# Optimization experiments

Measured on AMD Instinct MI355X. Metric: run time of the kernel, lower is better.

## Reference

```python
import jax, jax.numpy as jnp
import numpy as np

HEAD_NUM = 8
QKV_DIM = 16
EMB = 128
SQRT_EMB = 11.313708498984761  # sqrt(128)
LOGIT_CLIP = 10.0


def _heads(x):
    # (B, n, H*d) -> (B, H, n, d)
    B, n, _ = x.shape
    return x.reshape(B, n, HEAD_NUM, QKV_DIM).transpose(0, 2, 1, 3)


def _mha(q, k, v, rank3_ninf_mask):
    # q: (B,H,n,d), k/v: (B,H,m,d), mask: (B,n,m)
    score = jnp.einsum('bhnd,bhmd->bhnm', q, k) / jnp.sqrt(jnp.float32(QKV_DIM))
    score = score + rank3_ninf_mask[:, None, :, :]
    w = jax.nn.softmax(score, axis=3)
    out = jnp.einsum('bhnm,bhmd->bhnd', w, v)
    B, H, n, d = out.shape
    return out.transpose(0, 2, 1, 3).reshape(B, n, H * d)


def setup_inputs() -> dict:
    key = jax.random.key(0)
    ks = jax.random.split(key, 20)
    B, N, P = 32, 512, 512
    s = 1.0 / np.sqrt(EMB)
    inp = {
        'encoded_nodes': jax.random.normal(ks[0], (B, N, EMB), jnp.float32),
        'encoded_graph': jax.random.normal(ks[1], (B, N, EMB), jnp.float32),
        'encoded_q1': jax.random.normal(ks[2], (B, P, EMB), jnp.float32),
        'encoded_first_graph': jax.random.normal(ks[3], (B, P, EMB), jnp.float32),
        'encoded_last_node': jax.random.normal(ks[4], (B, P, EMB), jnp.float32),
        'encoded_last_graph': jax.random.normal(ks[5], (B, P, EMB), jnp.float32),
        'ninf_mask': jnp.zeros((B, P, N), jnp.float32),
        # weights stored (in, out); torch Linear y = x @ W.T
        'Wq_first': jax.random.uniform(ks[6], (EMB, EMB), jnp.float32, -s, s),
        'Wq_last': jax.random.uniform(ks[7], (EMB, EMB), jnp.float32, -s, s),
        'Wk': jax.random.uniform(ks[8], (EMB, EMB), jnp.float32, -s, s),
        'Wv': jax.random.uniform(ks[9], (EMB, EMB), jnp.float32, -s, s),
        'Wq_first_e': jax.random.uniform(ks[10], (EMB, EMB), jnp.float32, -s, s),
        'Wq_last_e': jax.random.uniform(ks[11], (EMB, EMB), jnp.float32, -s, s),
        'Wk_e': jax.random.uniform(ks[12], (EMB, EMB), jnp.float32, -s, s),
        'Wv_e': jax.random.uniform(ks[13], (EMB, EMB), jnp.float32, -s, s),
        'Wcomb1': jax.random.uniform(ks[14], (EMB, EMB), jnp.float32, -s, s),
        'bcomb1': jax.random.uniform(ks[15], (EMB,), jnp.float32, -s, s),
        'Wcomb2': jax.random.uniform(ks[16], (EMB, EMB), jnp.float32, -s, s),
        'bcomb2': jax.random.uniform(ks[17], (EMB,), jnp.float32, -s, s),
    }
    return inp


def reference(encoded_nodes, encoded_graph, encoded_q1, encoded_first_graph,
              encoded_last_node, encoded_last_graph, ninf_mask,
              Wq_first, Wq_last, Wk, Wv,
              Wq_first_e, Wq_last_e, Wk_e, Wv_e,
              Wcomb1, bcomb1, Wcomb2, bcomb2):
    # set_kv
    k = _heads(encoded_nodes @ Wk)
    v = _heads(encoded_nodes @ Wv)
    k_e = _heads(encoded_graph @ Wk_e)
    v_e = _heads(encoded_graph @ Wv_e)
    # set_q1
    q_first = _heads(encoded_q1 @ Wq_first)
    q_first_e = _heads(encoded_first_graph @ Wq_first_e)
    # forward
    q_last = _heads(encoded_last_node @ Wq_last)
    q_last_e = _heads(encoded_last_graph @ Wq_last_e)
    q = (q_first + q_last) + (q_first_e + q_last_e)
    out1 = _mha(q, k, v, ninf_mask)
    out2 = _mha(q, k_e, v_e, ninf_mask)
    mh_out = (out1 @ Wcomb1 + bcomb1) + (out2 @ Wcomb2 + bcomb2)
    # single-head scoring against summed keys: (B,n,e) x (B,N,e) -> (B,n,N)
    shk = encoded_nodes + encoded_graph
    score = jnp.einsum('bne,bNe->bnN', mh_out, shk) / SQRT_EMB
    score = LOGIT_CLIP * jnp.tanh(score) + ninf_mask
    probs = jax.nn.softmax(score, axis=2)
    return probs
```

## Files before the change

kernel.cpp:

```cpp
#include <hip/hip_runtime.h>

#define BATCH 32
#define SEQ   512
#define EMBD  128
#define HEADS 8
#define HD    16
#define ROWS  (BATCH*SEQ)
#define GR    32
#define NT32  (ROWS/GR)

__device__ __forceinline__ void gemm_nolds(const float* __restrict__ A,
                                           const float* __restrict__ W,
                                           int rowBase, int tid,
                                           float acc[4][4])
{
    const int r0 = (tid >> 5) * 4;
    const int c0 = (tid & 31) * 4;
    const float* Ab = A + (size_t)(rowBase + r0) * EMBD;
    for (int e0 = 0; e0 < EMBD; e0 += 4) {
        float4 a[4];
        #pragma unroll
        for (int r = 0; r < 4; ++r)
            a[r] = *(const float4*)(Ab + r*EMBD + e0);
        float4 w[4];
        #pragma unroll
        for (int j = 0; j < 4; ++j)
            w[j] = *(const float4*)(W + (e0+j)*EMBD + c0);
        #pragma unroll
        for (int r = 0; r < 4; ++r) {
            acc[r][0] += a[r].x*w[0].x + a[r].y*w[1].x + a[r].z*w[2].x + a[r].w*w[3].x;
            acc[r][1] += a[r].x*w[0].y + a[r].y*w[1].y + a[r].z*w[2].y + a[r].w*w[3].y;
            acc[r][2] += a[r].x*w[0].z + a[r].y*w[1].z + a[r].z*w[2].z + a[r].w*w[3].z;
            acc[r][3] += a[r].x*w[0].w + a[r].y*w[1].w + a[r].z*w[2].w + a[r].w*w[3].w;
        }
    }
}

__device__ __forceinline__ void store_nolds(float* __restrict__ out,
                                            int rowBase, int tid,
                                            float acc[4][4])
{
    const int r0 = (tid >> 5) * 4;
    const int c0 = (tid & 31) * 4;
    #pragma unroll
    for (int r = 0; r < 4; ++r)
        *(float4*)(out + (size_t)(rowBase + r0 + r)*EMBD + c0) =
            make_float4(acc[r][0], acc[r][1], acc[r][2], acc[r][3]);
}

__global__ __launch_bounds__(256) void proj_all_kernel(
    const float* __restrict__ nodes, const float* __restrict__ graph,
    const float* __restrict__ q1,    const float* __restrict__ fg,
    const float* __restrict__ ln,    const float* __restrict__ lg,
    const float* __restrict__ Wqf,  const float* __restrict__ Wql,
    const float* __restrict__ Wqfe, const float* __restrict__ Wqle,
    const float* __restrict__ Wk,   const float* __restrict__ Wv,
    const float* __restrict__ Wke,  const float* __restrict__ Wve,
    float* __restrict__ Qb, float* __restrict__ Kb, float* __restrict__ Vb,
    float* __restrict__ Keb, float* __restrict__ Veb)
{
    const int tid = threadIdx.x;
    const int rowBase = blockIdx.x * GR;
    const int job = blockIdx.y;
    float acc[4][4];
    #pragma unroll
    for (int r = 0; r < 4; ++r)
        #pragma unroll
        for (int c = 0; c < 4; ++c) acc[r][c] = 0.f;
    if (job == 0) {
        gemm_nolds(q1, Wqf,  rowBase, tid, acc);
        gemm_nolds(ln, Wql,  rowBase, tid, acc);
        gemm_nolds(fg, Wqfe, rowBase, tid, acc);
        gemm_nolds(lg, Wqle, rowBase, tid, acc);
        store_nolds(Qb, rowBase, tid, acc);
    } else if (job == 1) {
        gemm_nolds(nodes, Wk, rowBase, tid, acc);
        store_nolds(Kb, rowBase, tid, acc);
    } else if (job == 2) {
        gemm_nolds(nodes, Wv, rowBase, tid, acc);
        store_nolds(Vb, rowBase, tid, acc);
    } else if (job == 3) {
        gemm_nolds(graph, Wke, rowBase, tid, acc);
        store_nolds(Keb, rowBase, tid, acc);
    } else {
        gemm_nolds(graph, Wve, rowBase, tid, acc);
        store_nolds(Veb, rowBase, tid, acc);
    }
}

__global__ __launch_bounds__(256) void combine_kernel(
    const float* __restrict__ A0, const float* __restrict__ W0,
    const float* __restrict__ A1, const float* __restrict__ W1,
    const float* __restrict__ b0, const float* __restrict__ b1,
    float* __restrict__ out)
{
    const int tid = threadIdx.x;
    const int rowBase = blockIdx.x * GR;
    const int c0 = (tid & 31) * 4;
    float acc[4][4];
    #pragma unroll
    for (int c = 0; c < 4; ++c) {
        float bv = b0[c0+c] + b1[c0+c];
        #pragma unroll
        for (int r = 0; r < 4; ++r) acc[r][c] = bv;
    }
    gemm_nolds(A0, W0, rowBase, tid, acc);
    gemm_nolds(A1, W1, rowBase, tid, acc);
    store_nolds(out, rowBase, tid, acc);
}

__global__ __launch_bounds__(1024) void attn_kernel(
    const float* __restrict__ Qm, const float* __restrict__ Km,
    const float* __restrict__ Vm, const float* __restrict__ Kem,
    const float* __restrict__ Vem, const float* __restrict__ mask,
    float* __restrict__ out1, float* __restrict__ out2)
{
    extern __shared__ float smem[];
    float4* sK0 = (float4*)smem;
    float4* sV0 = sK0 + 2048;
    float4* sK1 = sV0 + 2048;
    float4* sV1 = sK1 + 2048;
    const int tid  = threadIdx.x;
    const int b    = blockIdx.x & 31;
    const int j    = blockIdx.x >> 5;
    const int type = j & 1;
    const int hp   = j >> 1;
    const float* K = type ? Kem : Km;
    const float* V = type ? Vem : Vm;
    float* outp    = type ? out2 : out1;
    const int h0 = hp * 2;
    {
        const float4* K4 = (const float4*)K;
        const float4* V4 = (const float4*)V;
        const int b0 = b*(SEQ*EMBD/4) + h0*(HD/4);
        #pragma unroll
        for (int k = 0; k < 2; ++k) {
            int i = tid + k*1024;
            int m = i >> 2, jj = i & 3;
            int g0 = b0 + m*(EMBD/4) + jj;
            sK0[i] = K4[g0];
            sV0[i] = V4[g0];
            sK1[i] = K4[g0 + 4];
            sV1[i] = V4[g0 + 4];
        }
    }
    __syncthreads();

    const int head = tid >> 9;
    const int row  = tid & 511;
    const float4* sK = head ? sK1 : sK0;
    const float4* sV = head ? sV1 : sV0;

    float q[16];
    {
        const float4* Q4 = (const float4*)Qm;
        const int qb = b*(SEQ*EMBD/4) + row*(EMBD/4) + (h0+head)*(HD/4);
        #pragma unroll
        for (int jj = 0; jj < 4; ++jj)
            *(float4*)&q[jj*4] = Q4[qb + jj];
    }
    const float4* mrow4 = (const float4*)(mask + ((size_t)b*SEQ + row)*SEQ);

    float l = 0.f;
    float acc[16];
    #pragma unroll
    for (int d = 0; d < 16; ++d) acc[d] = 0.f;

    for (int mc = 0; mc < SEQ/16; ++mc) {
        float4 mk[4];
        #pragma unroll
        for (int k = 0; k < 4; ++k) mk[k] = mrow4[mc*4 + k];
        const float* mkf = (const float*)mk;
        #pragma unroll
        for (int u = 0; u < 16; ++u) {
            const int m = mc*16 + u;
            float4 k0 = sK[m*4+0], k1 = sK[m*4+1], k2 = sK[m*4+2], k3 = sK[m*4+3];
            float s = q[0]*k0.x + q[1]*k0.y + q[2]*k0.z + q[3]*k0.w
                    + q[4]*k1.x + q[5]*k1.y + q[6]*k1.z + q[7]*k1.w
                    + q[8]*k2.x + q[9]*k2.y + q[10]*k2.z + q[11]*k2.w
                    + q[12]*k3.x + q[13]*k3.y + q[14]*k3.z + q[15]*k3.w;
            float p = __expf(s*0.25f + mkf[u]);
            l += p;
            float4 v0 = sV[m*4+0], v1 = sV[m*4+1], v2 = sV[m*4+2], v3 = sV[m*4+3];
            acc[0]+=p*v0.x;  acc[1]+=p*v0.y;  acc[2]+=p*v0.z;  acc[3]+=p*v0.w;
            acc[4]+=p*v1.x;  acc[5]+=p*v1.y;  acc[6]+=p*v1.z;  acc[7]+=p*v1.w;
            acc[8]+=p*v2.x;  acc[9]+=p*v2.y;  acc[10]+=p*v2.z; acc[11]+=p*v2.w;
            acc[12]+=p*v3.x; acc[13]+=p*v3.y; acc[14]+=p*v3.z; acc[15]+=p*v3.w;
        }
    }
    const float inv = 1.f / l;
    float4* o4 = (float4*)outp;
    const int ob = b*(SEQ*EMBD/4) + row*(EMBD/4) + (h0+head)*(HD/4);
    #pragma unroll
    for (int jj = 0; jj < 4; ++jj)
        o4[ob + jj] = make_float4(acc[jj*4]*inv, acc[jj*4+1]*inv,
                                  acc[jj*4+2]*inv, acc[jj*4+3]*inv);
}

#define RB 32
#define MT 64
__global__ __launch_bounds__(512) void final_kernel(
    const float* __restrict__ mh, const float* __restrict__ nodes,
    const float* __restrict__ graph, const float* __restrict__ mask,
    float* __restrict__ out)
{
    extern __shared__ float smem[];
    float4* sShk4 = (float4*)smem;
    float*  sMh   = smem + MT*EMBD;
    const int tid  = threadIdx.x;
    const int b    = blockIdx.x & 31;
    const int row0 = (blockIdx.x >> 5) * RB;
    const int mg = tid & 63;
    const int rg = tid >> 6;

    {
        const float4* mh4 = (const float4*)(mh + ((size_t)b*SEQ + row0)*EMBD);
        ((float4*)sMh)[tid]       = mh4[tid];
        ((float4*)sMh)[tid + 512] = mh4[tid + 512];
    }

    const float4* n4 = (const float4*)nodes;
    const float4* g4 = (const float4*)graph;
    float p[4][8];
    float rs[4] = {0.f, 0.f, 0.f, 0.f};

    #pragma unroll
    for (int mt = 0; mt < SEQ/MT; ++mt) {
        const int m0 = mt * MT;
        __syncthreads();
        {
            const int gb = (b*SEQ + m0) * (EMBD/4);
            #pragma unroll
            for (int k = 0; k < 4; ++k) {
                int i = tid + k*512;
                int m = i >> 5, f = i & 31;
                float4 x = n4[gb + m*32 + f];
                float4 y = g4[gb + m*32 + f];
                float4 s4;
                s4.x = x.x + y.x; s4.y = x.y + y.y;
                s4.z = x.z + y.z; s4.w = x.w + y.w;
                sShk4[(m << 5) | (f ^ (m & 31))] = s4;
            }
        }
        __syncthreads();

        float acc[4] = {0.f, 0.f, 0.f, 0.f};
        const int m = mg;
        #pragma unroll 8
        for (int e0 = 0; e0 < EMBD; e0 += 4) {
            const int f = e0 >> 2;
            float4 s = sShk4[(m << 5) | (f ^ (m & 31))];
            #pragma unroll
            for (int r = 0; r < 4; ++r) {
                const float* a = &sMh[(rg*4+r)*EMBD + e0];
                acc[r] += a[0]*s.x + a[1]*s.y + a[2]*s.z + a[3]*s.w;
            }
        }
        #pragma unroll
        for (int r = 0; r < 4; ++r) {
            const int row = row0 + rg*4 + r;
            float x = acc[r] * 0.088388347648318447f;
            float t = 1.f - 2.f / (__expf(2.f*x) + 1.f);
            float sc = 10.f*t + mask[((size_t)b*SEQ + row)*SEQ + m0 + mg];
            float pp = __expf(sc);
            p[r][mt] = pp;
            rs[r] += pp;
        }
    }

    #pragma unroll
    for (int r = 0; r < 4; ++r) {
        float s = rs[r];
        #pragma unroll
        for (int off = 32; off >= 1; off >>= 1) s += __shfl_xor(s, off);
        rs[r] = 1.f / s;
    }

    #pragma unroll
    for (int mt = 0; mt < SEQ/MT; ++mt) {
        #pragma unroll
        for (int r = 0; r < 4; ++r) {
            const int row = row0 + rg*4 + r;
            out[((size_t)b*SEQ + row)*SEQ + mt*MT + mg] = p[r][mt] * rs[r];
        }
    }
}

extern "C" void kernel_launch(void* const* d_in, const int* in_sizes, int n_in,
                              void* d_out, int out_size, void* d_ws, size_t ws_size,
                              hipStream_t stream)
{
    const float* nodes = (const float*)d_in[0];
    const float* graph = (const float*)d_in[1];
    const float* q1    = (const float*)d_in[2];
    const float* fg    = (const float*)d_in[3];
    const float* ln    = (const float*)d_in[4];
    const float* lg    = (const float*)d_in[5];
    const float* mask  = (const float*)d_in[6];
    const float* Wqf   = (const float*)d_in[7];
    const float* Wql   = (const float*)d_in[8];
    const float* Wk    = (const float*)d_in[9];
    const float* Wv    = (const float*)d_in[10];
    const float* Wqfe  = (const float*)d_in[11];
    const float* Wqle  = (const float*)d_in[12];
    const float* Wke   = (const float*)d_in[13];
    const float* Wve   = (const float*)d_in[14];
    const float* Wc1   = (const float*)d_in[15];
    const float* bc1   = (const float*)d_in[16];
    const float* Wc2   = (const float*)d_in[17];
    const float* bc2   = (const float*)d_in[18];

    float* ws = (float*)d_ws;
    const size_t BUF = (size_t)ROWS * EMBD;
    float* Qb  = ws;
    float* Kb  = ws + BUF;
    float* Vb  = ws + 2*BUF;
    float* Keb = ws + 3*BUF;
    float* Veb = ws + 4*BUF;
    float* mhb = Qb;
    float* o1  = (float*)d_out;
    float* o2  = o1 + BUF;

    const int LDS_ATTN  = 4 * SEQ * HD * 4;
    const int LDS_FINAL = (MT*EMBD + RB*EMBD) * 4;
    hipFuncSetAttribute((const void*)attn_kernel,  hipFuncAttributeMaxDynamicSharedMemorySize, LDS_ATTN);
    hipFuncSetAttribute((const void*)final_kernel, hipFuncAttributeMaxDynamicSharedMemorySize, LDS_FINAL);

    proj_all_kernel<<<dim3(NT32, 5), 256, 0, stream>>>(
        nodes, graph, q1, fg, ln, lg,
        Wqf, Wql, Wqfe, Wqle, Wk, Wv, Wke, Wve,
        Qb, Kb, Vb, Keb, Veb);
    attn_kernel<<<BATCH*8, 1024, LDS_ATTN, stream>>>(
        Qb, Kb, Vb, Keb, Veb, mask, o1, o2);
    combine_kernel<<<NT32, 256, 0, stream>>>(
        o1, Wc1, o2, Wc2, bc1, bc2, mhb);
    final_kernel<<<BATCH*(SEQ/RB), 512, LDS_FINAL, stream>>>(
        mhb, nodes, graph, mask, (float*)d_out);
}
```

Measured before the change: 547.7 us.

## Compute two query rows per thread in attention and two key columns in final

The attention kernel now runs 512 threads per block, and each thread handles two query rows, so every K/V value read from LDS is reused twice. The final kernel doubles its key tile to 128 and has each thread compute two key columns, so each mh value read from LDS is reused twice. Both changes cut LDS traffic per FLOP. The cost is roughly doubled accumulator registers and fewer threads per block in attention, which may reduce occupancy and latency hiding.

```diff
diff --git a/kernel.cpp b/kernel.cpp
--- a/kernel.cpp
+++ b/kernel.cpp
@@ -109,7 +109,7 @@
     store_nolds(out, rowBase, tid, acc);
 }
 
-__global__ __launch_bounds__(1024) void attn_kernel(
+__global__ __launch_bounds__(512) void attn_kernel(
     const float* __restrict__ Qm, const float* __restrict__ Km,
     const float* __restrict__ Vm, const float* __restrict__ Kem,
     const float* __restrict__ Vem, const float* __restrict__ mask,
@@ -134,8 +134,8 @@
         const float4* V4 = (const float4*)V;
         const int b0 = b*(SEQ*EMBD/4) + h0*(HD/4);
         #pragma unroll
-        for (int k = 0; k < 2; ++k) {
-            int i = tid + k*1024;
+        for (int k = 0; k < 4; ++k) {
+            int i = tid + k*512;
             int m = i >> 2, jj = i & 3;
             int g0 = b0 + m*(EMBD/4) + jj;
             sK0[i] = K4[g0];
@@ -146,59 +146,83 @@
     }
     __syncthreads();
 
-    const int head = tid >> 9;
-    const int row  = tid & 511;
+    const int head = tid >> 8;
+    const int r0   = tid & 255;
     const float4* sK = head ? sK1 : sK0;
     const float4* sV = head ? sV1 : sV0;
 
-    float q[16];
+    float q[2][16];
     {
         const float4* Q4 = (const float4*)Qm;
-        const int qb = b*(SEQ*EMBD/4) + row*(EMBD/4) + (h0+head)*(HD/4);
-        #pragma unroll
-        for (int jj = 0; jj < 4; ++jj)
-            *(float4*)&q[jj*4] = Q4[qb + jj];
-    }
-    const float4* mrow4 = (const float4*)(mask + ((size_t)b*SEQ + row)*SEQ);
-
-    float l = 0.f;
-    float acc[16];
-    #pragma unroll
-    for (int d = 0; d < 16; ++d) acc[d] = 0.f;
+        #pragma unroll
+        for (int rr = 0; rr < 2; ++rr) {
+            const int qb = b*(SEQ*EMBD/4) + (r0 + rr*256)*(EMBD/4) + (h0+head)*(HD/4);
+            #pragma unroll
+            for (int jj = 0; jj < 4; ++jj)
+                *(float4*)&q[rr][jj*4] = Q4[qb + jj];
+        }
+    }
+    const float4* mrowA = (const float4*)(mask + ((size_t)b*SEQ + r0)*SEQ);
+    const float4* mrowB = (const float4*)(mask + ((size_t)b*SEQ + r0 + 256)*SEQ);
+
+    float l0 = 0.f, l1 = 0.f;
+    float acc0[16], acc1[16];
+    #pragma unroll
+    for (int d = 0; d < 16; ++d) { acc0[d] = 0.f; acc1[d] = 0.f; }
 
     for (int mc = 0; mc < SEQ/16; ++mc) {
-        float4 mk[4];
-        #pragma unroll
-        for (int k = 0; k < 4; ++k) mk[k] = mrow4[mc*4 + k];
-        const float* mkf = (const float*)mk;
+        float4 mkA[4], mkB[4];
+        #pragma unroll
+        for (int k = 0; k < 4; ++k) { mkA[k] = mrowA[mc*4 + k]; mkB[k] = mrowB[mc*4 + k]; }
+        const float* mfA = (const float*)mkA;
+        const float* mfB = (const float*)mkB;
         #pragma unroll
         for (int u = 0; u < 16; ++u) {
             const int m = mc*16 + u;
             float4 k0 = sK[m*4+0], k1 = sK[m*4+1], k2 = sK[m*4+2], k3 = sK[m*4+3];
-            float s = q[0]*k0.x + q[1]*k0.y + q[2]*k0.z + q[3]*k0.w
-                    + q[4]*k1.x + q[5]*k1.y + q[6]*k1.z + q[7]*k1.w
-                    + q[8]*k2.x + q[9]*k2.y + q[10]*k2.z + q[11]*k2.w
-                    + q[12]*k3.x + q[13]*k3.y + q[14]*k3.z + q[15]*k3.w;
-            float p = __expf(s*0.25f + mkf[u]);
-            l += p;
+            float s0 = q[0][0]*k0.x + q[0][1]*k0.y + q[0][2]*k0.z + q[0][3]*k0.w
+                     + q[0][4]*k1.x + q[0][5]*k1.y + q[0][6]*k1.z + q[0][7]*k1.w
+                     + q[0][8]*k2.x + q[0][9]*k2.y + q[0][10]*k2.z + q[0][11]*k2.w
+                     + q[0][12]*k3.x + q[0][13]*k3.y + q[0][14]*k3.z + q[0][15]*k3.w;
+            float s1 = q[1][0]*k0.x + q[1][1]*k0.y + q[1][2]*k0.z + q[1][3]*k0.w
+                     + q[1][4]*k1.x + q[1][5]*k1.y + q[1][6]*k1.z + q[1][7]*k1.w
+                     + q[1][8]*k2.x + q[1][9]*k2.y + q[1][10]*k2.z + q[1][11]*k2.w
+                     + q[1][12]*k3.x + q[1][13]*k3.y + q[1][14]*k3.z + q[1][15]*k3.w;
+            float p0 = __expf(s0*0.25f + mfA[u]);
+            float p1 = __expf(s1*0.25f + mfB[u]);
+            l0 += p0; l1 += p1;
             float4 v0 = sV[m*4+0], v1 = sV[m*4+1], v2 = sV[m*4+2], v3 = sV[m*4+3];
-            acc[0]+=p*v0.x;  acc[1]+=p*v0.y;  acc[2]+=p*v0.z;  acc[3]+=p*v0.w;
-            acc[4]+=p*v1.x;  acc[5]+=p*v1.y;  acc[6]+=p*v1.z;  acc[7]+=p*v1.w;
-            acc[8]+=p*v2.x;  acc[9]+=p*v2.y;  acc[10]+=p*v2.z; acc[11]+=p*v2.w;
-            acc[12]+=p*v3.x; acc[13]+=p*v3.y; acc[14]+=p*v3.z; acc[15]+=p*v3.w;
-        }
-    }
-    const float inv = 1.f / l;
+            acc0[0]+=p0*v0.x;  acc0[1]+=p0*v0.y;  acc0[2]+=p0*v0.z;  acc0[3]+=p0*v0.w;
+            acc0[4]+=p0*v1.x;  acc0[5]+=p0*v1.y;  acc0[6]+=p0*v1.z;  acc0[7]+=p0*v1.w;
+            acc0[8]+=p0*v2.x;  acc0[9]+=p0*v2.y;  acc0[10]+=p0*v2.z; acc0[11]+=p0*v2.w;
+            acc0[12]+=p0*v3.x; acc0[13]+=p0*v3.y; acc0[14]+=p0*v3.z; acc0[15]+=p0*v3.w;
+            acc1[0]+=p1*v0.x;  acc1[1]+=p1*v0.y;  acc1[2]+=p1*v0.z;  acc1[3]+=p1*v0.w;
+            acc1[4]+=p1*v1.x;  acc1[5]+=p1*v1.y;  acc1[6]+=p1*v1.z;  acc1[7]+=p1*v1.w;
+            acc1[8]+=p1*v2.x;  acc1[9]+=p1*v2.y;  acc1[10]+=p1*v2.z; acc1[11]+=p1*v2.w;
+            acc1[12]+=p1*v3.x; acc1[13]+=p1*v3.y; acc1[14]+=p1*v3.z; acc1[15]+=p1*v3.w;
+        }
+    }
     float4* o4 = (float4*)outp;
-    const int ob = b*(SEQ*EMBD/4) + row*(EMBD/4) + (h0+head)*(HD/4);
-    #pragma unroll
-    for (int jj = 0; jj < 4; ++jj)
-        o4[ob + jj] = make_float4(acc[jj*4]*inv, acc[jj*4+1]*inv,
-                                  acc[jj*4+2]*inv, acc[jj*4+3]*inv);
+    const float i0 = 1.f / l0;
+    const float i1 = 1.f / l1;
+    {
+        const int ob = b*(SEQ*EMBD/4) + r0*(EMBD/4) + (h0+head)*(HD/4);
+        #pragma unroll
+        for (int jj = 0; jj < 4; ++jj)
+            o4[ob + jj] = make_float4(acc0[jj*4]*i0, acc0[jj*4+1]*i0,
+                                      acc0[jj*4+2]*i0, acc0[jj*4+3]*i0);
+    }
+    {
+        const int ob = b*(SEQ*EMBD/4) + (r0+256)*(EMBD/4) + (h0+head)*(HD/4);
+        #pragma unroll
+        for (int jj = 0; jj < 4; ++jj)
+            o4[ob + jj] = make_float4(acc1[jj*4]*i1, acc1[jj*4+1]*i1,
+                                      acc1[jj*4+2]*i1, acc1[jj*4+3]*i1);
+    }
 }
 
 #define RB 32
-#define MT 64
+#define MT 128
 __global__ __launch_bounds__(512) void final_kernel(
     const float* __restrict__ mh, const float* __restrict__ nodes,
     const float* __restrict__ graph, const float* __restrict__ mask,
@@ -231,7 +255,7 @@
         {
             const int gb = (b*SEQ + m0) * (EMBD/4);
             #pragma unroll
-            for (int k = 0; k < 4; ++k) {
+            for (int k = 0; k < 8; ++k) {
                 int i = tid + k*512;
                 int m = i >> 5, f = i & 31;
                 float4 x = n4[gb + m*32 + f];
@@ -244,27 +268,35 @@
         }
         __syncthreads();
 
-        float acc[4] = {0.f, 0.f, 0.f, 0.f};
-        const int m = mg;
+        float acc[4][2];
+        #pragma unroll
+        for (int r = 0; r < 4; ++r) { acc[r][0] = 0.f; acc[r][1] = 0.f; }
+        const int mA = mg, mB = mg + 64;
         #pragma unroll 8
         for (int e0 = 0; e0 < EMBD; e0 += 4) {
             const int f = e0 >> 2;
-            float4 s = sShk4[(m << 5) | (f ^ (m & 31))];
+            float4 s0 = sShk4[(mA << 5) | (f ^ (mA & 31))];
+            float4 s1 = sShk4[(mB << 5) | (f ^ (mB & 31))];
             #pragma unroll
             for (int r = 0; r < 4; ++r) {
                 const float* a = &sMh[(rg*4+r)*EMBD + e0];
-                acc[r] += a[0]*s.x + a[1]*s.y + a[2]*s.z + a[3]*s.w;
+                acc[r][0] += a[0]*s0.x + a[1]*s0.y + a[2]*s0.z + a[3]*s0.w;
+                acc[r][1] += a[0]*s1.x + a[1]*s1.y + a[2]*s1.z + a[3]*s1.w;
             }
         }
         #pragma unroll
         for (int r = 0; r < 4; ++r) {
             const int row = row0 + rg*4 + r;
-            float x = acc[r] * 0.088388347648318447f;
-            float t = 1.f - 2.f / (__expf(2.f*x) + 1.f);
-            float sc = 10.f*t + mask[((size_t)b*SEQ + row)*SEQ + m0 + mg];
-            float pp = __expf(sc);
-            p[r][mt] = pp;
-            rs[r] += pp;
+            const size_t mb = ((size_t)b*SEQ + row)*SEQ + m0;
+            #pragma unroll
+            for (int h = 0; h < 2; ++h) {
+                float x = acc[r][h] * 0.088388347648318447f;
+                float t = 1.f - 2.f / (__expf(2.f*x) + 1.f);
+                float sc = 10.f*t + mask[mb + h*64 + mg];
+                float pp = __expf(sc);
+                p[r][mt*2 + h] = pp;
+                rs[r] += pp;
+            }
         }
     }
 
@@ -281,7 +313,10 @@
         #pragma unroll
         for (int r = 0; r < 4; ++r) {
             const int row = row0 + rg*4 + r;
-            out[((size_t)b*SEQ + row)*SEQ + mt*MT + mg] = p[r][mt] * rs[r];
+            #pragma unroll
+            for (int h = 0; h < 2; ++h)
+                out[((size_t)b*SEQ + row)*SEQ + mt*MT + h*64 + mg] =
+                    p[r][mt*2 + h] * rs[r];
         }
     }
 }
@@ -330,7 +365,7 @@
         nodes, graph, q1, fg, ln, lg,
         Wqf, Wql, Wqfe, Wqle, Wk, Wv, Wke, Wve,
         Qb, Kb, Vb, Keb, Veb);
-    attn_kernel<<<BATCH*8, 1024, LDS_ATTN, stream>>>(
+    attn_kernel<<<BATCH*8, 512, LDS_ATTN, stream>>>(
         Qb, Kb, Vb, Keb, Veb, mask, o1, o2);
     combine_kernel<<<NT32, 256, 0, stream>>>(
         o1, Wc1, o2, Wc2, bc1, bc2, mhb);
```

Measured after the change: 557.7 us. About the same (+1.8%).

## Split attention key range across block halves and widen final-kernel tile

Applied to the files above, without the earlier changes.

Each attention block now processes a single head, with the two halves of the block handling opposite halves of the key sequence. Partial sums and exp totals are merged through shared memory. This halves LDS per block and doubles the grid, aiming for more resident blocks and better latency hiding. The Q scale is folded into q up front. The final scoring kernel computes two key columns per thread with a 128-key tile, which gives more reuse per LDS load but raises LDS use and may reduce occupancy.

```diff
diff --git a/kernel.cpp b/kernel.cpp
--- a/kernel.cpp
+++ b/kernel.cpp
@@ -109,77 +109,75 @@
     store_nolds(out, rowBase, tid, acc);
 }
 
-__global__ __launch_bounds__(1024) void attn_kernel(
+__global__ __launch_bounds__(1024, 8) void attn_kernel(
     const float* __restrict__ Qm, const float* __restrict__ Km,
     const float* __restrict__ Vm, const float* __restrict__ Kem,
     const float* __restrict__ Vem, const float* __restrict__ mask,
     float* __restrict__ out1, float* __restrict__ out2)
 {
     extern __shared__ float smem[];
-    float4* sK0 = (float4*)smem;
-    float4* sV0 = sK0 + 2048;
-    float4* sK1 = sV0 + 2048;
-    float4* sV1 = sK1 + 2048;
+    float4* sK = (float4*)smem;
+    float4* sV = sK + 2048;
+    float*  rL   = smem;
+    float*  rAcc = smem + 4096;
     const int tid  = threadIdx.x;
     const int b    = blockIdx.x & 31;
     const int j    = blockIdx.x >> 5;
     const int type = j & 1;
-    const int hp   = j >> 1;
+    const int h    = j >> 1;
     const float* K = type ? Kem : Km;
     const float* V = type ? Vem : Vm;
     float* outp    = type ? out2 : out1;
-    const int h0 = hp * 2;
     {
         const float4* K4 = (const float4*)K;
         const float4* V4 = (const float4*)V;
-        const int b0 = b*(SEQ*EMBD/4) + h0*(HD/4);
+        const int b0 = b*(SEQ*EMBD/4) + h*(HD/4);
         #pragma unroll
         for (int k = 0; k < 2; ++k) {
             int i = tid + k*1024;
             int m = i >> 2, jj = i & 3;
-            int g0 = b0 + m*(EMBD/4) + jj;
-            sK0[i] = K4[g0];
-            sV0[i] = V4[g0];
-            sK1[i] = K4[g0 + 4];
-            sV1[i] = V4[g0 + 4];
+            int g = b0 + m*(EMBD/4) + jj;
+            sK[i] = K4[g];
+            sV[i] = V4[g];
         }
     }
     __syncthreads();
 
-    const int head = tid >> 9;
+    const int half = tid >> 9;
     const int row  = tid & 511;
-    const float4* sK = head ? sK1 : sK0;
-    const float4* sV = head ? sV1 : sV0;
+    const int m0   = half * 256;
 
     float q[16];
     {
         const float4* Q4 = (const float4*)Qm;
-        const int qb = b*(SEQ*EMBD/4) + row*(EMBD/4) + (h0+head)*(HD/4);
+        const int qb = b*(SEQ*EMBD/4) + row*(EMBD/4) + h*(HD/4);
         #pragma unroll
         for (int jj = 0; jj < 4; ++jj)
             *(float4*)&q[jj*4] = Q4[qb + jj];
-    }
-    const float4* mrow4 = (const float4*)(mask + ((size_t)b*SEQ + row)*SEQ);
+        #pragma unroll
+        for (int d = 0; d < 16; ++d) q[d] *= 0.25f;
+    }
+    const float4* mrow4 = (const float4*)(mask + ((size_t)b*SEQ + row)*SEQ + m0);
 
     float l = 0.f;
     float acc[16];
     #pragma unroll
     for (int d = 0; d < 16; ++d) acc[d] = 0.f;
 
-    for (int mc = 0; mc < SEQ/16; ++mc) {
+    for (int mc = 0; mc < 16; ++mc) {
         float4 mk[4];
         #pragma unroll
         for (int k = 0; k < 4; ++k) mk[k] = mrow4[mc*4 + k];
         const float* mkf = (const float*)mk;
         #pragma unroll
         for (int u = 0; u < 16; ++u) {
-            const int m = mc*16 + u;
+            const int m = m0 + mc*16 + u;
             float4 k0 = sK[m*4+0], k1 = sK[m*4+1], k2 = sK[m*4+2], k3 = sK[m*4+3];
-            float s = q[0]*k0.x + q[1]*k0.y + q[2]*k0.z + q[3]*k0.w
-                    + q[4]*k1.x + q[5]*k1.y + q[6]*k1.z + q[7]*k1.w
-                    + q[8]*k2.x + q[9]*k2.y + q[10]*k2.z + q[11]*k2.w
-                    + q[12]*k3.x + q[13]*k3.y + q[14]*k3.z + q[15]*k3.w;
-            float p = __expf(s*0.25f + mkf[u]);
+            float sA = q[0]*k0.x + q[1]*k0.y + q[2]*k0.z + q[3]*k0.w;
+            float sB = q[4]*k1.x + q[5]*k1.y + q[6]*k1.z + q[7]*k1.w;
+            float sC = q[8]*k2.x + q[9]*k2.y + q[10]*k2.z + q[11]*k2.w;
+            float sD = q[12]*k3.x + q[13]*k3.y + q[14]*k3.z + q[15]*k3.w;
+            float p = __expf((sA + sB) + (sC + sD) + mkf[u]);
             l += p;
             float4 v0 = sV[m*4+0], v1 = sV[m*4+1], v2 = sV[m*4+2], v3 = sV[m*4+3];
             acc[0]+=p*v0.x;  acc[1]+=p*v0.y;  acc[2]+=p*v0.z;  acc[3]+=p*v0.w;
@@ -188,17 +186,30 @@
             acc[12]+=p*v3.x; acc[13]+=p*v3.y; acc[14]+=p*v3.z; acc[15]+=p*v3.w;
         }
     }
-    const float inv = 1.f / l;
-    float4* o4 = (float4*)outp;
-    const int ob = b*(SEQ*EMBD/4) + row*(EMBD/4) + (h0+head)*(HD/4);
-    #pragma unroll
-    for (int jj = 0; jj < 4; ++jj)
-        o4[ob + jj] = make_float4(acc[jj*4]*inv, acc[jj*4+1]*inv,
-                                  acc[jj*4+2]*inv, acc[jj*4+3]*inv);
+
+    __syncthreads();
+    if (half) {
+        rL[row] = l;
+        #pragma unroll
+        for (int d = 0; d < 16; ++d) rAcc[row*17 + d] = acc[d];
+    }
+    __syncthreads();
+    if (!half) {
+        l += rL[row];
+        #pragma unroll
+        for (int d = 0; d < 16; ++d) acc[d] += rAcc[row*17 + d];
+        const float inv = 1.f / l;
+        float4* o4 = (float4*)outp;
+        const int ob = b*(SEQ*EMBD/4) + row*(EMBD/4) + h*(HD/4);
+        #pragma unroll
+        for (int jj = 0; jj < 4; ++jj)
+            o4[ob + jj] = make_float4(acc[jj*4]*inv, acc[jj*4+1]*inv,
+                                      acc[jj*4+2]*inv, acc[jj*4+3]*inv);
+    }
 }
 
 #define RB 32
-#define MT 64
+#define MT 128
 __global__ __launch_bounds__(512) void final_kernel(
     const float* __restrict__ mh, const float* __restrict__ nodes,
     const float* __restrict__ graph, const float* __restrict__ mask,
@@ -231,7 +242,7 @@
         {
             const int gb = (b*SEQ + m0) * (EMBD/4);
             #pragma unroll
-            for (int k = 0; k < 4; ++k) {
+            for (int k = 0; k < 8; ++k) {
                 int i = tid + k*512;
                 int m = i >> 5, f = i & 31;
                 float4 x = n4[gb + m*32 + f];
@@ -244,27 +255,35 @@
         }
         __syncthreads();
 
-        float acc[4] = {0.f, 0.f, 0.f, 0.f};
-        const int m = mg;
+        float acc[4][2];
+        #pragma unroll
+        for (int r = 0; r < 4; ++r) { acc[r][0] = 0.f; acc[r][1] = 0.f; }
+        const int mA = mg, mB = mg + 64;
         #pragma unroll 8
         for (int e0 = 0; e0 < EMBD; e0 += 4) {
             const int f = e0 >> 2;
-            float4 s = sShk4[(m << 5) | (f ^ (m & 31))];
+            float4 s0 = sShk4[(mA << 5) | (f ^ (mA & 31))];
+            float4 s1 = sShk4[(mB << 5) | (f ^ (mB & 31))];
             #pragma unroll
             for (int r = 0; r < 4; ++r) {
                 const float* a = &sMh[(rg*4+r)*EMBD + e0];
-                acc[r] += a[0]*s.x + a[1]*s.y + a[2]*s.z + a[3]*s.w;
+                acc[r][0] += a[0]*s0.x + a[1]*s0.y + a[2]*s0.z + a[3]*s0.w;
+                acc[r][1] += a[0]*s1.x + a[1]*s1.y + a[2]*s1.z + a[3]*s1.w;
             }
         }
         #pragma unroll
         for (int r = 0; r < 4; ++r) {
             const int row = row0 + rg*4 + r;
-            float x = acc[r] * 0.088388347648318447f;
-            float t = 1.f - 2.f / (__expf(2.f*x) + 1.f);
-            float sc = 10.f*t + mask[((size_t)b*SEQ + row)*SEQ + m0 + mg];
-            float pp = __expf(sc);
-            p[r][mt] = pp;
-            rs[r] += pp;
+            const size_t mb = ((size_t)b*SEQ + row)*SEQ + m0;
+            #pragma unroll
+            for (int h = 0; h < 2; ++h) {
+                float x = acc[r][h] * 0.088388347648318447f;
+                float t = 1.f - 2.f / (__expf(2.f*x) + 1.f);
+                float sc = 10.f*t + mask[mb + h*64 + mg];
+                float pp = __expf(sc);
+                p[r][mt*2 + h] = pp;
+                rs[r] += pp;
+            }
         }
     }
 
@@ -281,7 +300,10 @@
         #pragma unroll
         for (int r = 0; r < 4; ++r) {
             const int row = row0 + rg*4 + r;
-            out[((size_t)b*SEQ + row)*SEQ + mt*MT + mg] = p[r][mt] * rs[r];
+            #pragma unroll
+            for (int h = 0; h < 2; ++h)
+                out[((size_t)b*SEQ + row)*SEQ + mt*MT + h*64 + mg] =
+                    p[r][mt*2 + h] * rs[r];
         }
     }
 }
@@ -321,7 +343,7 @@
     float* o1  = (float*)d_out;
     float* o2  = o1 + BUF;
 
-    const int LDS_ATTN  = 4 * SEQ * HD * 4;
+    const int LDS_ATTN  = 2 * SEQ * HD * 4;
     const int LDS_FINAL = (MT*EMBD + RB*EMBD) * 4;
     hipFuncSetAttribute((const void*)attn_kernel,  hipFuncAttributeMaxDynamicSharedMemorySize, LDS_ATTN);
     hipFuncSetAttribute((const void*)final_kernel, hipFuncAttributeMaxDynamicSharedMemorySize, LDS_FINAL);
@@ -330,7 +352,7 @@
         nodes, graph, q1, fg, ln, lg,
         Wqf, Wql, Wqfe, Wqle, Wk, Wv, Wke, Wve,
         Qb, Kb, Vb, Keb, Veb);
-    attn_kernel<<<BATCH*8, 1024, LDS_ATTN, stream>>>(
+    attn_kernel<<<BATCH*16, 1024, LDS_ATTN, stream>>>(
         Qb, Kb, Vb, Keb, Veb, mask, o1, o2);
     combine_kernel<<<NT32, 256, 0, stream>>>(
         o1, Wc1, o2, Wc2, bc1, bc2, mhb);
```

Measured after the change: 1.196 ms. 2.18x slower.
